# Kernel tuning notes

Measured on AMD Instinct MI355X. Metric: run time of the kernel, lower is better.

## Reference

```python
import jax, jax.numpy as jnp
import numpy as np

B, C, H, W = 8, 1024, 32, 32   # batch, in_channels (cnn==vit), spatial
OUT = 2048                     # out_channels
NHEAD = 32                     # heads -> head_dim 64
EMBED_DIM = 1024               # used ONLY for the softmax scale (faithful to source)
LN_EPS = 1e-5


def setup_inputs() -> dict:
    key = jax.random.key(0)
    ks = jax.random.split(key, 8)
    f = lambda k, s: jax.random.normal(k, s, dtype=jnp.float32)
    return {
        "x_cnn": f(ks[0], (B, C, H, W)),
        "x_vit": f(ks[1], (B, C, H, W)),
        "Wq": f(ks[2], (OUT, C)) * 0.02, "bq": jnp.zeros((OUT,), jnp.float32),
        "Wk": f(ks[3], (OUT, C)) * 0.02, "bk": jnp.zeros((OUT,), jnp.float32),
        "Wv": f(ks[4], (OUT, C)) * 0.02, "bv": jnp.zeros((OUT,), jnp.float32),
        "w_mix": jnp.float32(0.5),
        "ln_g": jnp.ones((OUT,), jnp.float32), "ln_b": jnp.zeros((OUT,), jnp.float32),
        "Wfc": f(ks[5], (OUT, OUT)) * 0.02, "bfc": jnp.zeros((OUT,), jnp.float32),
    }


def _mha(Q, K, V):
    # Q,K,V: [b, n, OUT] -> multi-head attention, scale by sqrt(EMBED_DIM) as in source
    b, n, _ = Q.shape
    d = OUT // NHEAD
    Qh = Q.reshape(b, n, NHEAD, d)
    Kh = K.reshape(b, n, NHEAD, d)
    Vh = V.reshape(b, n, NHEAD, d)
    scores = jnp.einsum('bqhd,bkhd->bhqk', Qh, Kh) / jnp.sqrt(jnp.float32(EMBED_DIM))
    attn = jax.nn.softmax(scores, axis=-1)
    out = jnp.einsum('bhqk,bkhd->bqhd', attn, Vh)
    return out.reshape(b, n, OUT)


def reference(x_cnn, x_vit, Wq, bq, Wk, bk, Wv, bv, w_mix, ln_g, ln_b, Wfc, bfc):
    b, c, h, w = x_cnn.shape
    xc = x_cnn.reshape(b, c, h * w).transpose(0, 2, 1)   # [b, hw, c]
    xv = x_vit.reshape(b, c, h * w).transpose(0, 2, 1)
    # shared projections, two cross directions
    Q1 = xc @ Wq.T + bq; K1 = xv @ Wk.T + bk; V1 = xv @ Wv.T + bv
    Q2 = xv @ Wq.T + bq; K2 = xc @ Wk.T + bk; V2 = xc @ Wv.T + bv
    attended_vit = _mha(Q1, K1, V1)   # cnn queries attend vit
    attended_cnn = _mha(Q2, K2, V2)   # vit queries attend cnn
    r = attended_cnn * w_mix + attended_vit * (1.0 - w_mix)
    # LayerNorm over last dim (population variance, like torch)
    mu = jnp.mean(r, axis=-1, keepdims=True)
    var = jnp.var(r, axis=-1, keepdims=True)
    r = (r - mu) / jnp.sqrt(var + LN_EPS) * ln_g + ln_b
    r = r @ Wfc.T + bfc
    return r.transpose(0, 2, 1).reshape(b, OUT, h, w)
```

## Files before the change

### kernel.cpp

```cpp
#include <hip/hip_runtime.h>
#include <stdint.h>

typedef unsigned short u16;
typedef unsigned int u32;
typedef __attribute__((ext_vector_type(4))) float float4v;
typedef __attribute__((ext_vector_type(4))) unsigned int uint4v;
typedef __attribute__((ext_vector_type(4))) unsigned short u16x4;
typedef __attribute__((ext_vector_type(8))) short s16x8;
typedef __attribute__((ext_vector_type(4))) float f32x4;

__device__ __forceinline__ float bf2f(u16 h) {
    union { u32 u; float f; } v; v.u = ((u32)h) << 16; return v.f;
}
__device__ __forceinline__ u16 f2bf(float f) {
    union { float f; u32 u; } v; v.f = f;
    u32 r = (v.u + 0x7fffu + ((v.u >> 16) & 1u)) >> 16;
    return (u16)r;
}

__device__ __forceinline__ bool detect_f32(const u16* lng) {
    return *(const u32*)lng == 0x3F800000u;
}

__device__ __forceinline__ float read_wmix(const void* wmix) {
    u32 word = *(const u32*)wmix;
    if ((word & 0xFFFFu) == 0u) {
        union { u32 u; float f; } v; v.u = word; return v.f;
    }
    return bf2f((u16)(word & 0xFFFFu));
}

__device__ __forceinline__ uint4v load8(const void* base, long long off, bool isF32) {
    if (isF32) {
        const float* p = (const float*)base + off;
        float4v f0 = *(const float4v*)p;
        float4v f1 = *(const float4v*)(p + 4);
        uint4v r; u16* h = (u16*)&r;
#pragma unroll
        for (int i = 0; i < 4; ++i) { h[i] = f2bf(f0[i]); h[4 + i] = f2bf(f1[i]); }
        return r;
    }
    return *(const uint4v*)((const u16*)base + off);
}
__device__ __forceinline__ float loadraw(const void* p, int idx, bool isF32) {
    return isF32 ? ((const float*)p)[idx] : bf2f(((const u16*)p)[idx]);
}

__global__ __launch_bounds__(256) void convert_w(
    const void* __restrict__ src, u16* __restrict__ dst, int n,
    const u16* __restrict__ lng)
{
    bool f32 = detect_f32(lng);
    long long i = ((long long)blockIdx.x * 256 + threadIdx.x) * 8;
    if (i >= n) return;
    uint4v v = load8(src, i, f32);
    *(uint4v*)(dst + i) = v;
}

__global__ __launch_bounds__(256) void transpose_k(
    const void* __restrict__ xc, const void* __restrict__ xv,
    u16* __restrict__ xt, const u16* __restrict__ lng)
{
    bool f32 = detect_f32(lng);
    int z = blockIdx.z;
    const void* xbase = (z < 8 ? xc : xv);
    long long soff = (long long)(z & 7) * 1024 * 1024;
    u16* outp = xt + (long long)z * 1024 * 1024;
    int c0 = blockIdx.x * 64, p0 = blockIdx.y * 64;
    __shared__ u16 t[64][72];
    int tid = threadIdx.x;
    int cl = tid >> 3, ch = tid & 7;
#pragma unroll
    for (int pass = 0; pass < 2; ++pass) {
        int c = cl + pass * 32;
        uint4v v = load8(xbase, soff + (long long)(c0 + c) * 1024 + p0 + ch * 8, f32);
        const u16* vv = (const u16*)&v;
#pragma unroll
        for (int i = 0; i < 8; ++i) t[ch * 8 + i][c] = vv[i];
    }
    __syncthreads();
#pragma unroll
    for (int pass = 0; pass < 2; ++pass) {
        int p = cl + pass * 32;
        uint4v v; u16* vv = (u16*)&v;
#pragma unroll
        for (int i = 0; i < 8; ++i) vv[i] = t[p][ch * 8 + i];
        *(uint4v*)(outp + (long long)(p0 + p) * 1024 + c0 + ch * 8) = v;
    }
}

__global__ __launch_bounds__(256) void transpose_v(
    const u16* __restrict__ V, u16* __restrict__ VT)
{
    int b = blockIdx.z, head = blockIdx.y, p0 = blockIdx.x * 64;
    const u16* src = V + (long long)b * 1024 * 2048 + head * 64;
    u16* dst = VT + (long long)(b * 32 + head) * 64 * 1024;
    __shared__ u16 t[64][72];
    int tid = threadIdx.x;
    int r = tid >> 3, ch = tid & 7;
#pragma unroll
    for (int pass = 0; pass < 2; ++pass) {
        int p = r + pass * 32;
        uint4v v = *(const uint4v*)(src + (long long)(p0 + p) * 2048 + ch * 8);
        const u16* vv = (const u16*)&v;
#pragma unroll
        for (int i = 0; i < 8; ++i) t[ch * 8 + i][p] = vv[i];
    }
    __syncthreads();
#pragma unroll
    for (int pass = 0; pass < 2; ++pass) {
        int d = r + pass * 32;
        uint4v v = *(const uint4v*)&t[d][ch * 8];
        *(uint4v*)(dst + (long long)d * 1024 + p0 + ch * 8) = v;
    }
}

__global__ __launch_bounds__(256) void gemm_mfma(
    const void* __restrict__ A, int lda, long long sA, int a_raw,
    const void* __restrict__ B, int ldb, long long sB, int b_raw,
    const void* __restrict__ bias,
    void* __restrict__ Cv, int ldc, long long sC, int c_f32,
    int K, int bias_on_m, const u16* __restrict__ lng)
{
    bool f32 = detect_f32(lng);
    bool aF = f32 && a_raw, bF = f32 && b_raw;
    int z = blockIdx.z;
    long long aoff = (long long)z * sA, boff = (long long)z * sB;
    long long coff = (long long)z * sC;
    int m0 = blockIdx.x * 128, n0 = blockIdx.y * 128;
    int tid = threadIdx.x;
    int lane = tid & 63, wave = tid >> 6;
    int lrow = lane & 15, lgrp = lane >> 4;
    int wm = (wave >> 1) * 64, wn = (wave & 1) * 64;

    __shared__ u16 As[128][72];
    __shared__ u16 Bs[128][72];

    f32x4 acc[4][4];
#pragma unroll
    for (int i = 0; i < 4; ++i)
#pragma unroll
        for (int j = 0; j < 4; ++j) acc[i][j] = (f32x4)0.f;

    int sr = tid >> 3;
    int kc = (tid & 7) * 8;

    long long arow[4], brow[4];
#pragma unroll
    for (int q = 0; q < 4; ++q) {
        arow[q] = aoff + (long long)(m0 + sr + q * 32) * lda;
        brow[q] = boff + (long long)(n0 + sr + q * 32) * ldb;
    }

    uint4v an[4], bn[4];
#pragma unroll
    for (int q = 0; q < 4; ++q) {
        an[q] = load8(A, arow[q] + kc, aF);
        bn[q] = load8(B, brow[q] + kc, bF);
    }

    for (int k0 = 0; k0 < K; k0 += 64) {
        uint4v ac[4], bc[4];
#pragma unroll
        for (int q = 0; q < 4; ++q) { ac[q] = an[q]; bc[q] = bn[q]; }
        __syncthreads();
#pragma unroll
        for (int q = 0; q < 4; ++q) {
            *(uint4v*)&As[sr + q * 32][kc] = ac[q];
            *(uint4v*)&Bs[sr + q * 32][kc] = bc[q];
        }
        __syncthreads();
        if (k0 + 64 < K) {
#pragma unroll
            for (int q = 0; q < 4; ++q) {
                an[q] = load8(A, arow[q] + k0 + 64 + kc, aF);
                bn[q] = load8(B, brow[q] + k0 + 64 + kc, bF);
            }
        }
#pragma unroll
        for (int kk = 0; kk < 2; ++kk) {
            s16x8 af[4], bfr[4];
#pragma unroll
            for (int i = 0; i < 4; ++i)
                af[i] = *(const s16x8*)&As[wm + i * 16 + lrow][kk * 32 + lgrp * 8];
#pragma unroll
            for (int j = 0; j < 4; ++j)
                bfr[j] = *(const s16x8*)&Bs[wn + j * 16 + lrow][kk * 32 + lgrp * 8];
#pragma unroll
            for (int i = 0; i < 4; ++i)
#pragma unroll
                for (int j = 0; j < 4; ++j)
                    acc[i][j] = __builtin_amdgcn_mfma_f32_16x16x32_bf16(
                        af[i], bfr[j], acc[i][j], 0, 0, 0);
        }
    }

    float bnj[4];
#pragma unroll
    for (int j = 0; j < 4; ++j)
        bnj[j] = bias_on_m ? 0.f : loadraw(bias, n0 + wn + j * 16 + lrow, f32);
#pragma unroll
    for (int i = 0; i < 4; ++i) {
#pragma unroll
        for (int e = 0; e < 4; ++e) {
            int mrow = m0 + wm + i * 16 + lgrp * 4 + e;
            float bm = bias_on_m ? loadraw(bias, mrow, f32) : 0.f;
#pragma unroll
            for (int j = 0; j < 4; ++j) {
                int ncol = n0 + wn + j * 16 + lrow;
                float val = acc[i][j][e] + (bias_on_m ? bm : bnj[j]);
                long long idx = coff + (long long)mrow * ldc + ncol;
                if (c_f32) ((float*)Cv)[idx] = val;
                else       ((u16*)Cv)[idx] = f2bf(val);
            }
        }
    }
}

__global__ __launch_bounds__(256) void attn_mfma(
    u16* __restrict__ Qb, const u16* __restrict__ Kb, const u16* __restrict__ VTb)
{
    const int ld = 2048;
    int bz = blockIdx.z, head = blockIdx.y;
    int q0 = blockIdx.x * 64;
    long long base = (long long)bz * 1024 * ld + head * 64;
    u16* Q = Qb + base;
    const u16* K = Kb + base;
    const u16* VT = VTb + (long long)(bz * 32 + head) * 64 * 1024;

    int tid = threadIdx.x;
    int wave = tid >> 6, lane = tid & 63;
    int lrow = lane & 15, lgrp = lane >> 4;

    __shared__ u16 Kt[64][72];
    __shared__ u16 VTt[64][72];
    __shared__ u16 Pt[4][16][72];

    int qw = q0 + wave * 16;
    s16x8 qf0, qf1;
    {
        const u16* qp = Q + (long long)(qw + lrow) * ld + lgrp * 8;
        qf0 = *(const s16x8*)qp;
        qf1 = *(const s16x8*)(qp + 32);
    }

    f32x4 of[4];
#pragma unroll
    for (int dt = 0; dt < 4; ++dt) of[dt] = (f32x4)0.f;
    float m_run = -1e30f, l_run = 0.f;

    for (int t = 0; t < 16; ++t) {
        int k0 = t * 64;
        {
            int key = tid >> 2, ch = tid & 3;
#pragma unroll
            for (int pass = 0; pass < 2; ++pass) {
                int c = ch * 8 + pass * 32;
                *(uint4v*)&Kt[key][c] =
                    *(const uint4v*)(K + (long long)(k0 + key) * ld + c);
            }
        }
        {
            int d = tid >> 2, off = (tid & 3) * 16;
            const u16* vp = VT + (long long)d * 1024 + k0 + off;
            *(uint4v*)&VTt[d][off]     = *(const uint4v*)vp;
            *(uint4v*)&VTt[d][off + 8] = *(const uint4v*)(vp + 8);
        }
        __syncthreads();

        f32x4 sf[4];
#pragma unroll
        for (int f = 0; f < 4; ++f) {
            s16x8 kf0 = *(const s16x8*)&Kt[f * 16 + lrow][lgrp * 8];
            s16x8 kf1 = *(const s16x8*)&Kt[f * 16 + lrow][lgrp * 8 + 32];
            f32x4 acc = (f32x4)0.f;
            acc = __builtin_amdgcn_mfma_f32_16x16x32_bf16(kf0, qf0, acc, 0, 0, 0);
            acc = __builtin_amdgcn_mfma_f32_16x16x32_bf16(kf1, qf1, acc, 0, 0, 0);
#pragma unroll
            for (int i = 0; i < 4; ++i) acc[i] *= 0.03125f;
            sf[f] = acc;
        }

        float mx = sf[0][0];
#pragma unroll
        for (int f = 0; f < 4; ++f)
#pragma unroll
            for (int i = 0; i < 4; ++i) mx = fmaxf(mx, sf[f][i]);
        mx = fmaxf(mx, __shfl_xor(mx, 16));
        mx = fmaxf(mx, __shfl_xor(mx, 32));
        float m_new = fmaxf(m_run, mx);
        float sc = __expf(m_run - m_new);
        float p[4][4], rs = 0.f;
#pragma unroll
        for (int f = 0; f < 4; ++f)
#pragma unroll
            for (int i = 0; i < 4; ++i) {
                p[f][i] = __expf(sf[f][i] - m_new);
                rs += p[f][i];
            }
        rs += __shfl_xor(rs, 16);
        rs += __shfl_xor(rs, 32);
        l_run = l_run * sc + rs;
        m_run = m_new;
#pragma unroll
        for (int dt = 0; dt < 4; ++dt)
#pragma unroll
            for (int i = 0; i < 4; ++i) of[dt][i] *= sc;

#pragma unroll
        for (int f = 0; f < 4; ++f) {
            u16x4 pk;
#pragma unroll
            for (int i = 0; i < 4; ++i) pk[i] = f2bf(p[f][i]);
            *(u16x4*)&Pt[wave][lrow][f * 16 + lgrp * 4] = pk;
        }
        asm volatile("s_waitcnt lgkmcnt(0)" ::: "memory");

#pragma unroll
        for (int kk = 0; kk < 2; ++kk) {
            s16x8 pb = *(const s16x8*)&Pt[wave][lrow][kk * 32 + lgrp * 8];
#pragma unroll
            for (int dt = 0; dt < 4; ++dt) {
                s16x8 va = *(const s16x8*)&VTt[dt * 16 + lrow][kk * 32 + lgrp * 8];
                of[dt] = __builtin_amdgcn_mfma_f32_16x16x32_bf16(va, pb, of[dt], 0, 0, 0);
            }
        }
        __syncthreads();
    }

    float linv = 1.f / l_run;
#pragma unroll
    for (int dt = 0; dt < 4; ++dt) {
        u16x4 o;
#pragma unroll
        for (int i = 0; i < 4; ++i) o[i] = f2bf(of[dt][i] * linv);
        *(u16x4*)(Q + (long long)(qw + lrow) * ld + dt * 16 + lgrp * 4) = o;
    }
}

__global__ __launch_bounds__(256) void mix_ln_k(
    const u16* __restrict__ Avit, const u16* __restrict__ Acnn,
    const void* __restrict__ wmix,
    const void* __restrict__ g, const void* __restrict__ bta,
    u16* __restrict__ Y, const u16* __restrict__ lng)
{
    bool f32 = detect_f32(lng);
    long long row = blockIdx.x;
    const u16* a0 = Avit + row * 2048;
    const u16* a1 = Acnn + row * 2048;
    int tid = threadIdx.x, lane = tid & 63, wave = tid >> 6;
    float w = read_wmix(wmix);
    int o = tid * 8;
    uint4v x0 = *(const uint4v*)(a0 + o);
    uint4v x1 = *(const uint4v*)(a1 + o);
    const u16* p0 = (const u16*)&x0;
    const u16* p1 = (const u16*)&x1;
    float r[8], sum = 0.f, sq = 0.f;
#pragma unroll
    for (int e = 0; e < 8; ++e) {
        r[e] = w * bf2f(p1[e]) + (1.f - w) * bf2f(p0[e]);
        sum += r[e]; sq += r[e] * r[e];
    }
#pragma unroll
    for (int off = 1; off < 64; off <<= 1) {
        sum += __shfl_xor(sum, off);
        sq += __shfl_xor(sq, off);
    }
    __shared__ float red[8];
    if (lane == 0) { red[wave] = sum; red[4 + wave] = sq; }
    __syncthreads();
    sum = red[0] + red[1] + red[2] + red[3];
    sq = red[4] + red[5] + red[6] + red[7];
    float mu = sum * (1.f / 2048.f);
    float var = sq * (1.f / 2048.f) - mu * mu;
    float rstd = rsqrtf(var + 1e-5f);
    uint4v y; u16* py = (u16*)&y;
#pragma unroll
    for (int e = 0; e < 8; ++e)
        py[e] = f2bf((r[e] - mu) * rstd * loadraw(g, o + e, f32) + loadraw(bta, o + e, f32));
    *(uint4v*)(Y + row * 2048 + o) = y;
}

extern "C" void kernel_launch(void* const* d_in, const int* in_sizes, int n_in,
                              void* d_out, int out_size, void* d_ws, size_t ws_size,
                              hipStream_t stream)
{
    const void* x_cnn = d_in[0];
    const void* x_vit = d_in[1];
    const void* Wq = d_in[2];
    const void* bq = d_in[3];
    const void* Wk = d_in[4];
    const void* bk = d_in[5];
    const void* Wv = d_in[6];
    const void* bv = d_in[7];
    const void* wmix = d_in[8];
    const u16* ln_g = (const u16*)d_in[9];
    const void* ln_b = d_in[10];
    const void* Wfc = d_in[11];
    const void* bfc = d_in[12];

    u16* X   = (u16*)d_out;
    u16* VTb = (u16*)((char*)d_out + 33554432);
    char* ws = (char*)d_ws;
    u16* S0 = (u16*)ws;
    u16* S1 = (u16*)(ws + 1LL * 33554432);
    u16* S2 = (u16*)(ws + 2LL * 33554432);
    u16* S3 = (u16*)(ws + 3LL * 33554432);
    const long long SRC = 8LL * 1024 * 1024;

    const long long WS4 = 4LL * 33554432;
    bool tail = ws_size >= (size_t)(WS4 + 20971520LL);
    u16* WqB = (u16*)(ws + WS4);
    u16* WkB = WqB + 2097152;
    u16* WvB = WkB + 2097152;
    u16* WfB = WvB + 2097152;
    if (tail) {
        convert_w<<<1024, 256, 0, stream>>>(Wq, WqB, 2097152, ln_g);
        convert_w<<<1024, 256, 0, stream>>>(Wk, WkB, 2097152, ln_g);
        convert_w<<<1024, 256, 0, stream>>>(Wv, WvB, 2097152, ln_g);
        convert_w<<<2048, 256, 0, stream>>>(Wfc, WfB, 4194304, ln_g);
    }
    const void* pWq = tail ? (const void*)WqB : Wq;
    const void* pWk = tail ? (const void*)WkB : Wk;
    const void* pWv = tail ? (const void*)WvB : Wv;
    const void* pWf = tail ? (const void*)WfB : Wfc;
    int rawW = tail ? 0 : 1;

    transpose_k<<<dim3(16, 16, 16), 256, 0, stream>>>(x_cnn, x_vit, X, ln_g);

    dim3 pg(64, 16, 1);
    gemm_mfma<<<pg, 256, 0, stream>>>(X,       1024, 0LL, 0, pWq, 1024, 0LL, rawW, bq,
                                      S0, 2048, 0LL, 0, 1024, 0, ln_g);
    gemm_mfma<<<pg, 256, 0, stream>>>(X + SRC, 1024, 0LL, 0, pWk, 1024, 0LL, rawW, bk,
                                      S1, 2048, 0LL, 0, 1024, 0, ln_g);
    gemm_mfma<<<pg, 256, 0, stream>>>(X + SRC, 1024, 0LL, 0, pWv, 1024, 0LL, rawW, bv,
                                      S2, 2048, 0LL, 0, 1024, 0, ln_g);
    transpose_v<<<dim3(16, 32, 8), 256, 0, stream>>>(S2, VTb);
    attn_mfma<<<dim3(16, 32, 8), 256, 0, stream>>>(S0, S1, VTb);

    gemm_mfma<<<pg, 256, 0, stream>>>(X + SRC, 1024, 0LL, 0, pWq, 1024, 0LL, rawW, bq,
                                      S1, 2048, 0LL, 0, 1024, 0, ln_g);
    gemm_mfma<<<pg, 256, 0, stream>>>(X,       1024, 0LL, 0, pWk, 1024, 0LL, rawW, bk,
                                      S2, 2048, 0LL, 0, 1024, 0, ln_g);
    gemm_mfma<<<pg, 256, 0, stream>>>(X,       1024, 0LL, 0, pWv, 1024, 0LL, rawW, bv,
                                      S3, 2048, 0LL, 0, 1024, 0, ln_g);
    transpose_v<<<dim3(16, 32, 8), 256, 0, stream>>>(S3, VTb);
    attn_mfma<<<dim3(16, 32, 8), 256, 0, stream>>>(S1, S2, VTb);

    mix_ln_k<<<8192, 256, 0, stream>>>(S0, S1, wmix, ln_g, ln_b, S2, ln_g);

    gemm_mfma<<<dim3(16, 8, 8), 256, 0, stream>>>(pWf, 2048, 0LL, rawW, S2, 2048, 1024LL * 2048, 0, bfc,
                                                  d_out, 1024, 2048LL * 1024, 1, 2048, 1, ln_g);
}
```

Baseline: 935.4 us.

## Prefetch K/V tiles, use exp2 lazy-rescale softmax, and swizzle block order

The attention kernel now prefetches the next K/VT tile into registers while the current tile is computed. It folds the 1/32 score scale and log2(e) into a single exp2 (v_exp_f32) and rescales the running max only when it grows by more than 8 in the log2 domain. Both the GEMM and attention kernels remap workgroup IDs with an 8-way swizzle, intended to improve cache locality across XCDs. The bf16 rounding drops round-to-nearest-even for a cheaper round-half-up, which slightly changes numerics. The lazy rescale lets exp values reach up to 2^8 before correction, which raises rounding-error risk in bf16 P.

```diff
diff --git a/kernel.cpp b/kernel.cpp
--- a/kernel.cpp
+++ b/kernel.cpp
@@ -14,8 +14,10 @@
 }
 __device__ __forceinline__ u16 f2bf(float f) {
     union { float f; u32 u; } v; v.f = f;
-    u32 r = (v.u + 0x7fffu + ((v.u >> 16) & 1u)) >> 16;
-    return (u16)r;
+    return (u16)((v.u + 0x8000u) >> 16);
+}
+__device__ __forceinline__ float exp2_fast(float x) {
+    float r; asm("v_exp_f32 %0, %1" : "=v"(r) : "v"(x)); return r;
 }
 
 __device__ __forceinline__ bool detect_f32(const u16* lng) {
@@ -124,10 +126,16 @@
 {
     bool f32 = detect_f32(lng);
     bool aF = f32 && a_raw, bF = f32 && b_raw;
-    int z = blockIdx.z;
+    int gx = gridDim.x, gy = gridDim.y, gz = gridDim.z;
+    int flat = blockIdx.x + gx * (blockIdx.y + gy * blockIdx.z);
+    int nwg = gx * gy * gz;
+    int wsw = ((nwg & 7) == 0) ? ((flat & 7) * (nwg >> 3) + (flat >> 3)) : flat;
+    int bxi = wsw % gx, rem = wsw / gx;
+    int byi = rem % gy, z = rem / gy;
+
     long long aoff = (long long)z * sA, boff = (long long)z * sB;
     long long coff = (long long)z * sC;
-    int m0 = blockIdx.x * 128, n0 = blockIdx.y * 128;
+    int m0 = bxi * 128, n0 = byi * 128;
     int tid = threadIdx.x;
     int lane = tid & 63, wave = tid >> 6;
     int lrow = lane & 15, lgrp = lane >> 4;
@@ -221,8 +229,11 @@
     u16* __restrict__ Qb, const u16* __restrict__ Kb, const u16* __restrict__ VTb)
 {
     const int ld = 2048;
-    int bz = blockIdx.z, head = blockIdx.y;
-    int q0 = blockIdx.x * 64;
+    const float SCL = 0.0450985123f;
+    int flat = blockIdx.x + 16 * (blockIdx.y + 32 * blockIdx.z);
+    int w = (flat & 7) * 512 + (flat >> 3);
+    int qt = w & 15, head = (w >> 4) & 31, bz = w >> 9;
+    int q0 = qt * 64;
     long long base = (long long)bz * 1024 * ld + head * 64;
     u16* Q = Qb + base;
     const u16* K = Kb + base;
@@ -247,24 +258,28 @@
     f32x4 of[4];
 #pragma unroll
     for (int dt = 0; dt < 4; ++dt) of[dt] = (f32x4)0.f;
-    float m_run = -1e30f, l_run = 0.f;
+    float mL = 0.f, l_run = 0.f;
+
+    int skey = tid >> 2, sc4 = tid & 3;
+    const u16* kptr = K + (long long)skey * ld + sc4 * 8;
+    const u16* vptr = VT + (long long)skey * 1024 + sc4 * 16;
+    uint4v ka0 = *(const uint4v*)kptr;
+    uint4v ka1 = *(const uint4v*)(kptr + 32);
+    uint4v va0 = *(const uint4v*)vptr;
+    uint4v va1 = *(const uint4v*)(vptr + 8);
 
     for (int t = 0; t < 16; ++t) {
-        int k0 = t * 64;
-        {
-            int key = tid >> 2, ch = tid & 3;
-#pragma unroll
-            for (int pass = 0; pass < 2; ++pass) {
-                int c = ch * 8 + pass * 32;
-                *(uint4v*)&Kt[key][c] =
-                    *(const uint4v*)(K + (long long)(k0 + key) * ld + c);
-            }
-        }
-        {
-            int d = tid >> 2, off = (tid & 3) * 16;
-            const u16* vp = VT + (long long)d * 1024 + k0 + off;
-            *(uint4v*)&VTt[d][off]     = *(const uint4v*)vp;
-            *(uint4v*)&VTt[d][off + 8] = *(const uint4v*)(vp + 8);
+        *(uint4v*)&Kt[skey][sc4 * 8]       = ka0;
+        *(uint4v*)&Kt[skey][sc4 * 8 + 32]  = ka1;
+        *(uint4v*)&VTt[skey][sc4 * 16]     = va0;
+        *(uint4v*)&VTt[skey][sc4 * 16 + 8] = va1;
+        if (t < 15) {
+            kptr += 64 * ld;
+            vptr += 64;
+            ka0 = *(const uint4v*)kptr;
+            ka1 = *(const uint4v*)(kptr + 32);
+            va0 = *(const uint4v*)vptr;
+            va1 = *(const uint4v*)(vptr + 8);
         }
         __syncthreads();
 
@@ -273,12 +288,10 @@
         for (int f = 0; f < 4; ++f) {
             s16x8 kf0 = *(const s16x8*)&Kt[f * 16 + lrow][lgrp * 8];
             s16x8 kf1 = *(const s16x8*)&Kt[f * 16 + lrow][lgrp * 8 + 32];
-            f32x4 acc = (f32x4)0.f;
-            acc = __builtin_amdgcn_mfma_f32_16x16x32_bf16(kf0, qf0, acc, 0, 0, 0);
-            acc = __builtin_amdgcn_mfma_f32_16x16x32_bf16(kf1, qf1, acc, 0, 0, 0);
-#pragma unroll
-            for (int i = 0; i < 4; ++i) acc[i] *= 0.03125f;
-            sf[f] = acc;
+            f32x4 a = (f32x4)0.f;
+            a = __builtin_amdgcn_mfma_f32_16x16x32_bf16(kf0, qf0, a, 0, 0, 0);
+            a = __builtin_amdgcn_mfma_f32_16x16x32_bf16(kf1, qf1, a, 0, 0, 0);
+            sf[f] = a;
         }
 
         float mx = sf[0][0];
@@ -288,33 +301,34 @@
             for (int i = 0; i < 4; ++i) mx = fmaxf(mx, sf[f][i]);
         mx = fmaxf(mx, __shfl_xor(mx, 16));
         mx = fmaxf(mx, __shfl_xor(mx, 32));
-        float m_new = fmaxf(m_run, mx);
-        float sc = __expf(m_run - m_new);
-        float p[4][4], rs = 0.f;
-#pragma unroll
-        for (int f = 0; f < 4; ++f)
+        if (__any(mx * SCL > mL + 8.f)) {
+            float mLn = fmaxf(mL, mx * SCL);
+            float sc = exp2_fast(mL - mLn);
+            l_run *= sc;
+#pragma unroll
+            for (int dt = 0; dt < 4; ++dt)
+#pragma unroll
+                for (int i = 0; i < 4; ++i) of[dt][i] *= sc;
+            mL = mLn;
+        }
+
+        float nmL = -mL, rs = 0.f;
+#pragma unroll
+        for (int f = 0; f < 4; ++f) {
+            u16x4 pk;
 #pragma unroll
             for (int i = 0; i < 4; ++i) {
-                p[f][i] = __expf(sf[f][i] - m_new);
-                rs += p[f][i];
+                float pe = exp2_fast(fmaf(sf[f][i], SCL, nmL));
+                rs += pe;
+                pk[i] = f2bf(pe);
             }
+            *(u16x4*)&Pt[wave][lrow][f * 16 + lgrp * 4] = pk;
+        }
         rs += __shfl_xor(rs, 16);
         rs += __shfl_xor(rs, 32);
-        l_run = l_run * sc + rs;
-        m_run = m_new;
-#pragma unroll
-        for (int dt = 0; dt < 4; ++dt)
-#pragma unroll
-            for (int i = 0; i < 4; ++i) of[dt][i] *= sc;
-
-#pragma unroll
-        for (int f = 0; f < 4; ++f) {
-            u16x4 pk;
-#pragma unroll
-            for (int i = 0; i < 4; ++i) pk[i] = f2bf(p[f][i]);
-            *(u16x4*)&Pt[wave][lrow][f * 16 + lgrp * 4] = pk;
-        }
+        l_run += rs;
         asm volatile("s_waitcnt lgkmcnt(0)" ::: "memory");
+        __builtin_amdgcn_sched_barrier(0);
 
 #pragma unroll
         for (int kk = 0; kk < 2; ++kk) {
```

Measured after the change: 924.1 us. About the same (-1.2%).
